# Kernel optimization log

Measured on AMD Instinct MI355X. Metric: run time of the kernel, lower is better.

The kernel has to match this reference:

```python
import jax, jax.numpy as jnp
import numpy as np

N_NODES = 100_000
N_EDGES = 1_600_000
N_SPECIES = 4
ATTR = 16
HID = 32
NBASIS = 8
SH = 4  # l=0 (1) + l=1 (3)
R_CUT = 5.0


def setup_inputs() -> dict:
    key = jax.random.key(0)
    ks = jax.random.split(key, 13)
    inp = {
        "x": jax.random.randint(ks[0], (N_NODES,), 0, N_SPECIES),
        "pos": jax.random.normal(ks[1], (N_NODES, 3), jnp.float32),
        "edge_index": jax.random.randint(ks[2], (2, N_EDGES), 0, N_NODES),
        "cell": jax.random.normal(ks[3], (3, 3), jnp.float32),
        "cell_offset": jax.random.randint(ks[4], (N_EDGES, 3), 0, 3),
        "elem_embed": jax.random.normal(ks[5], (N_SPECIES, ATTR), jnp.float32),
        "W_embed": jax.random.normal(ks[6], (ATTR, HID), jnp.float32) * 0.25,
        "Wr": jax.random.normal(ks[7], (3, NBASIS, HID * SH), jnp.float32) * 0.25,
        "br": jax.random.normal(ks[8], (3, HID * SH), jnp.float32) * 0.1,
        "Wout": jax.random.normal(ks[9], (3, HID, HID), jnp.float32) * 0.18,
        "Wsc": jax.random.normal(ks[10], (3, ATTR, HID), jnp.float32) * 0.25,
        "P1": jax.random.normal(ks[11], (HID, 32), jnp.float32) * 0.18,
        "P2": jax.random.normal(ks[12], (32, 4), jnp.float32) * 0.18,
    }
    return inp


def _radial_basis(r, r_safe):
    # Bessel basis with smooth polynomial cutoff (p = 6)
    n = jnp.arange(1, NBASIS + 1, dtype=r.dtype)  # [NBASIS]
    rb = jnp.sin(n * jnp.pi * r / R_CUT) / r_safe  # [E, NBASIS]
    u = r / R_CUT
    p = 6.0
    env = 1.0 - (p + 1) * (p + 2) / 2 * u ** p + p * (p + 2) * u ** (p + 1) - p * (p + 1) / 2 * u ** (p + 2)
    env = jnp.where(u < 1.0, env, 0.0)
    return rb * env


def reference(x, pos, edge_index, cell, cell_offset, elem_embed, W_embed, Wr, br, Wout, Wsc, P1, P2):
    src, dst = edge_index[0], edge_index[1]
    n_nodes = pos.shape[0]
    n_edges = src.shape[0]

    # PBC shift vectors (offsets in {-1,0,1})
    period_vec = (cell_offset.astype(pos.dtype) - 1.0) @ cell  # [E,3]

    # node attributes / initial embedding
    x_attr = elem_embed[x]          # [N, ATTR]
    h = x_attr @ W_embed            # [N, HID]

    # edge attributes: vectors, lengths, spherical harmonics (l<=1)
    edge_vec = pos[dst] - pos[src] + period_vec            # [E,3]
    r = jnp.linalg.norm(edge_vec, axis=-1, keepdims=True)  # [E,1]
    r_safe = jnp.maximum(r, 1e-9)
    unit = edge_vec / r_safe
    edge_sh = jnp.concatenate([jnp.ones_like(r), unit], axis=-1)  # [E,SH]

    rbf = _radial_basis(r, r_safe)  # [E, NBASIS]

    # 3 message-passing convolutions
    for l in range(3):
        w = (rbf @ Wr[l] + br[l]).reshape(n_edges, HID, SH)          # per-edge TP weights
        msg = jnp.einsum('eh,es,ehs->eh', h[src], edge_sh, w)        # gather + edge compute
        agg = jax.ops.segment_sum(msg, dst, num_segments=n_nodes)    # scatter-reduce
        h = jax.nn.silu(agg @ Wout[l] + x_attr @ Wsc[l])

    # post-conv readout
    h = jax.nn.silu(h @ P1) @ P2  # [N,4]
    energies = h[:, 0]
    forces = h[:, 1:4]
    return energies, forces
```

## Files before the change

kernel.cpp:

```cpp
#include <hip/hip_runtime.h>
#include <hip/hip_bf16.h>
#include <math.h>

#define NN 100000
#define NE 1600000
#define HIDD 32
#define ATTR_ 16
#define NB 8
#define NBUK 782
#define BCAP 4096
#define SCHUNK 4096

typedef __hip_bfloat16 bf16;
typedef _Float16 half8  __attribute__((ext_vector_type(8)));
typedef _Float16 half2v __attribute__((ext_vector_type(2)));
typedef float    f32x4  __attribute__((ext_vector_type(4)));

__device__ __forceinline__ float silu_(float v){ return v / (1.f + expf(-v)); }

__global__ void k_init(const int* __restrict__ x, const float* __restrict__ elem,
                       const float* __restrict__ Wemb, bf16* __restrict__ h,
                       float* __restrict__ agg){
  int idx = blockIdx.x*256 + threadIdx.x;
  if (idx >= NN*HIDD) return;
  int node = idx >> 5, hh = idx & 31;
  int xi = x[node];
  float acc = 0.f;
  #pragma unroll
  for (int a=0; a<ATTR_; a++) acc += elem[xi*ATTR_+a] * Wemb[a*HIDD+hh];
  h[idx] = __float2bfloat16(acc);
  agg[idx] = 0.f;
}

__global__ void k_bzero(int* __restrict__ bcnt){
  int i = blockIdx.x*1024 + threadIdx.x;
  if (i < NBUK) bcnt[i] = 0;
}

__global__ void __launch_bounds__(256) k_bhist(const int* __restrict__ ei,
                                               int* __restrict__ bcnt){
  __shared__ int lh[NBUK];
  const int t = threadIdx.x;
  for (int i=t; i<NBUK; i+=256) lh[i] = 0;
  __syncthreads();
  const size_t base = (size_t)blockIdx.x * 8192;
  #pragma unroll
  for (int k=0; k<32; k++){
    size_t e = base + (size_t)k*256 + t;
    if (e < NE) atomicAdd(&lh[ei[NE + e] >> 7], 1);
  }
  __syncthreads();
  for (int i=t; i<NBUK; i+=256){ int v = lh[i]; if (v) atomicAdd(&bcnt[i], v); }
}

__global__ void __launch_bounds__(1024) k_bscan(const int* __restrict__ bcnt,
                                                int* __restrict__ boff,
                                                int* __restrict__ bcur){
  __shared__ int s[1024];
  const int t = threadIdx.x;
  int v = (t < NBUK) ? bcnt[t] : 0;
  s[t] = v; __syncthreads();
  #pragma unroll
  for (int off=1; off<1024; off<<=1){
    int u = (t >= off) ? s[t-off] : 0;
    __syncthreads();
    s[t] += u;
    __syncthreads();
  }
  int ex = s[t] - v;
  if (t < NBUK){ boff[t] = ex; bcur[t] = ex; }
  if (t == NBUK-1) boff[NBUK] = s[t];
}

__global__ void __launch_bounds__(256) k_bscatter(
    const int* __restrict__ ei, const int* __restrict__ coff,
    int* __restrict__ bcur, int* __restrict__ pairs){
  __shared__ int lh[NBUK];
  __shared__ int gb[NBUK];
  __shared__ int sbr[SCHUNK];
  __shared__ int spay[SCHUNK];
  const int t = threadIdx.x;
  const int base = blockIdx.x * SCHUNK;
  for (int i=t; i<NBUK; i+=256) lh[i] = 0;
  __syncthreads();
  for (int rr=0; rr<SCHUNK; rr+=256){
    int e = base + rr + t;
    if (e < NE){
      int src = ei[e], dst = ei[NE + e];
      int code = coff[e*3+0] + 3*coff[e*3+1] + 9*coff[e*3+2];
      int b = dst >> 7;
      int rank = atomicAdd(&lh[b], 1);
      sbr[rr+t]  = (b<<16) | rank;
      spay[rr+t] = src | (code<<17) | ((dst & 127)<<22);
    }
  }
  __syncthreads();
  for (int i=t; i<NBUK; i+=256){
    int c = lh[i];
    gb[i] = c ? atomicAdd(&bcur[i], c) : 0;
  }
  __syncthreads();
  for (int rr=0; rr<SCHUNK; rr+=256){
    int e = base + rr + t;
    if (e < NE){
      int br = sbr[rr+t];
      pairs[gb[br>>16] + (br & 0xFFFF)] = spay[rr+t];
    }
  }
}

__global__ void __launch_bounds__(256) k_fsort(
    const int* __restrict__ pairs, const int* __restrict__ boff,
    int* __restrict__ es, int* __restrict__ dsts){
  __shared__ int spay[BCAP];
  __shared__ int hist[128];
  __shared__ int cur[128];
  const int b = blockIdx.x, t = threadIdx.x;
  const int base = boff[b];
  int K = boff[b+1] - base;
  if (K > BCAP) K = BCAP;
  if (t < 128) hist[t] = 0;
  __syncthreads();
  for (int i=t; i<K; i+=256){
    int pay = pairs[base + i];
    spay[i] = pay;
    atomicAdd(&hist[(pay>>22) & 127], 1);
  }
  __syncthreads();
  if (t < 128) cur[t] = hist[t];
  __syncthreads();
  #pragma unroll
  for (int off=1; off<128; off<<=1){
    int u = (t >= off && t < 128) ? cur[t-off] : 0;
    __syncthreads();
    if (t < 128) cur[t] += u;
    __syncthreads();
  }
  if (t < 128) cur[t] -= hist[t];
  __syncthreads();
  const int node0 = b << 7;
  for (int i=t; i<K; i+=256){
    int pay = spay[i];
    int loc = (pay>>22) & 127;
    int p = base + atomicAdd(&cur[loc], 1);
    es[p]   = pay;
    dsts[p] = node0 + loc;
  }
}

__global__ void __launch_bounds__(256) k_edge4(
    const int* __restrict__ es, const int* __restrict__ dsts,
    const float* __restrict__ pos, const float* __restrict__ cell,
    const float* __restrict__ Wr_l, const float* __restrict__ br_l,
    const bf16* __restrict__ h, float* __restrict__ agg){
  __shared__ _Float16 Gs[256][40];
  __shared__ float ssh[256][4];
  __shared__ int ssrc[256];
  __shared__ int sdst[256];
  __shared__ _Float16 W2T[32][32];
  __shared__ float scell[9];
  const int t = threadIdx.x;
  if (t < 9) scell[t] = cell[t];
  {
    int hh2 = t >> 3, kq = t & 7;
    float4 w4 = *reinterpret_cast<const float4*>(Wr_l + kq*128 + hh2*4);
    W2T[hh2][kq*4+0] = (_Float16)w4.x;
    W2T[hh2][kq*4+1] = (_Float16)w4.y;
    W2T[hh2][kq*4+2] = (_Float16)w4.z;
    W2T[hh2][kq*4+3] = (_Float16)w4.w;
  }
  __syncthreads();

  {
    const int j = blockIdx.x*256 + t;
    int pay = es[j];
    int dst = dsts[j];
    int src  = pay & 0x1FFFF;
    int code = (pay >> 17) & 31;
    ssrc[t] = src; sdst[t] = dst;
    int q = code / 3;
    float c0 = (float)(code - 3*q - 1);
    float c1 = (float)(q - 3*(q/3) - 1);
    float c2 = (float)(q/3 - 1);
    float vx = pos[dst*3+0]-pos[src*3+0] + c0*scell[0]+c1*scell[3]+c2*scell[6];
    float vy = pos[dst*3+1]-pos[src*3+1] + c0*scell[1]+c1*scell[4]+c2*scell[7];
    float vz = pos[dst*3+2]-pos[src*3+2] + c0*scell[2]+c1*scell[5]+c2*scell[8];
    float r  = sqrtf(vx*vx + vy*vy + vz*vz);
    float rs = fmaxf(r, 1e-9f);
    float u  = r * 0.2f;
    float env = 0.f;
    if (u < 1.f){
      float u2=u*u, u3=u2*u, u6=u3*u3, u7=u6*u, u8=u7*u;
      env = 1.f - 28.f*u6 + 48.f*u7 - 21.f*u8;
    }
    float sc = env / rs;
    float s1, c1t;
    __sincosf(0.62831853071795864769f * r, &s1, &c1t);
    float twoc = 2.f*c1t;
    float inv = 1.f / rs;
    float ux = vx*inv, uy = vy*inv, uz = vz*inv;
    float sp = 0.f, sn = s1;
    #pragma unroll
    for (int b=0; b<NB; b++){
      float rb = sn*sc;
      half2v p0 = { (_Float16)rb,      (_Float16)(rb*ux) };
      half2v p1 = { (_Float16)(rb*uy), (_Float16)(rb*uz) };
      *reinterpret_cast<half2v*>(&Gs[t][b*4])   = p0;
      *reinterpret_cast<half2v*>(&Gs[t][b*4+2]) = p1;
      float nx = twoc*sn - sp; sp = sn; sn = nx;
    }
    float4 sh4 = make_float4(1.f, ux, uy, uz);
    *reinterpret_cast<float4*>(ssh[t]) = sh4;
  }
  __syncthreads();

  {
    const int w = t >> 6, l = t & 63;
    const int lrow = l & 15, lk = l >> 4;
    half8 b0 = *reinterpret_cast<half8*>(&W2T[lrow][lk*8]);
    half8 b1 = *reinterpret_cast<half8*>(&W2T[16+lrow][lk*8]);
    float4 br0 = *reinterpret_cast<const float4*>(br_l + 4*lrow);
    float4 br1 = *reinterpret_cast<const float4*>(br_l + 4*(16+lrow));
    f32x4 acc[4][2];
    const f32x4 zz = {0.f,0.f,0.f,0.f};
    #pragma unroll
    for (int m=0; m<4; m++){
      int row = (w*4+m)*16 + lrow;
      half8 a = *reinterpret_cast<half8*>(&Gs[row][lk*8]);
      acc[m][0] = __builtin_amdgcn_mfma_f32_16x16x32_f16(a, b0, zz, 0, 0, 0);
      acc[m][1] = __builtin_amdgcn_mfma_f32_16x16x32_f16(a, b1, zz, 0, 0, 0);
    }
    #pragma unroll
    for (int m=0; m<4; m++){
      #pragma unroll
      for (int r=0; r<4; r++){
        int edge = (w*4+m)*16 + lk*4 + r;
        float4 sh4 = *reinterpret_cast<float4*>(ssh[edge]);
        float bias0 = sh4.x*br0.x + sh4.y*br0.y + sh4.z*br0.z + sh4.w*br0.w;
        float bias1 = sh4.x*br1.x + sh4.y*br1.y + sh4.z*br1.z + sh4.w*br1.w;
        Gs[edge][lrow]    = (_Float16)(acc[m][0][r] + bias0);
        Gs[edge][16+lrow] = (_Float16)(acc[m][1][r] + bias1);
      }
    }
  }
  __syncthreads();

  const int g = t >> 5, hh = t & 31, base = g*32;
  float accv = 0.f;
  int cur = sdst[base];
  float buf[16];
  #pragma unroll
  for (int half = 0; half < 2; half++){
    const int kb = base + half*16;
    #pragma unroll
    for (int k=0; k<16; k++)
      buf[k] = __bfloat162float(h[(size_t)ssrc[kb+k]*HIDD + hh]);
    #pragma unroll
    for (int k=0; k<16; k++){
      const int idx = kb + k;
      int dst = sdst[idx];
      if (dst != cur){ atomicAdd(agg + (size_t)cur*HIDD + hh, accv); accv = 0.f; cur = dst; }
      float cv = (float)Gs[idx][hh];
      accv += buf[k]*cv;
    }
  }
  atomicAdd(agg + (size_t)cur*HIDD + hh, accv);
}

__global__ void __launch_bounds__(256) k_edge(
    const float* __restrict__ pos, const int* __restrict__ ei,
    const float* __restrict__ cell, const int* __restrict__ coff,
    const float* __restrict__ Wr_l, const float* __restrict__ br_l,
    const bf16* __restrict__ h, float* __restrict__ agg){
  __shared__ float sfeat[8][12];
  __shared__ int   snode[8][2];
  const int e0 = blockIdx.x * 8;
  const int t  = threadIdx.x;
  if (t < 8){
    int e = e0 + t;
    int src = ei[e], dst = ei[NE + e];
    snode[t][0] = src; snode[t][1] = dst;
    float c0 = (float)(coff[e*3+0] - 1);
    float c1 = (float)(coff[e*3+1] - 1);
    float c2 = (float)(coff[e*3+2] - 1);
    float vx = pos[dst*3+0]-pos[src*3+0] + c0*cell[0]+c1*cell[3]+c2*cell[6];
    float vy = pos[dst*3+1]-pos[src*3+1] + c0*cell[1]+c1*cell[4]+c2*cell[7];
    float vz = pos[dst*3+2]-pos[src*3+2] + c0*cell[2]+c1*cell[5]+c2*cell[8];
    float r  = sqrtf(vx*vx+vy*vy+vz*vz);
    float rs = fmaxf(r, 1e-9f);
    float u  = r * 0.2f;
    float env = 0.f;
    if (u < 1.f){
      float u2=u*u, u3=u2*u, u6=u3*u3, u7=u6*u, u8=u7*u;
      env = 1.f - 28.f*u6 + 48.f*u7 - 21.f*u8;
    }
    float sc = env / rs;
    #pragma unroll
    for (int b=0; b<NB; b++)
      sfeat[t][b] = sinf((float)(b+1) * 3.14159265358979323846f * u) * sc;
    float inv = 1.f / rs;
    sfeat[t][8]  = 1.f;
    sfeat[t][9]  = vx*inv;
    sfeat[t][10] = vy*inv;
    sfeat[t][11] = vz*inv;
  }
  __syncthreads();
  const int el = t >> 5, hh = t & 31;
  const int src = snode[el][0], dst = snode[el][1];
  float hs = __bfloat162float(h[(size_t)src*HIDD + hh]);
  float4 acc = *reinterpret_cast<const float4*>(br_l + 4*hh);
  #pragma unroll
  for (int b=0; b<NB; b++){
    float rb = sfeat[el][b];
    float4 w = *reinterpret_cast<const float4*>(Wr_l + b*128 + 4*hh);
    acc.x += rb*w.x; acc.y += rb*w.y; acc.z += rb*w.z; acc.w += rb*w.w;
  }
  float c = acc.x*sfeat[el][8] + acc.y*sfeat[el][9]
          + acc.z*sfeat[el][10] + acc.w*sfeat[el][11];
  atomicAdd(agg + (size_t)dst*HIDD + hh, hs*c);
}

__global__ void k_node(const int* __restrict__ x, const float* __restrict__ elem,
                       const float* __restrict__ Wout_l, const float* __restrict__ Wsc_l,
                       bf16* __restrict__ h, float* __restrict__ agg){
  int idx = blockIdx.x*256 + threadIdx.x;
  if (idx >= NN*HIDD) return;
  int node = idx >> 5, hh = idx & 31;
  int xi = x[node];
  const float* arow = agg + (size_t)node*HIDD;
  float acc = 0.f;
  #pragma unroll
  for (int i=0; i<HIDD; i++) acc += arow[i] * Wout_l[i*HIDD+hh];
  #pragma unroll
  for (int a=0; a<ATTR_; a++) acc += elem[xi*ATTR_+a] * Wsc_l[a*HIDD+hh];
  h[idx] = __float2bfloat16(silu_(acc));
  agg[idx] = 0.f;
}

__global__ void __launch_bounds__(256) k_final2(
    const bf16* __restrict__ h, const float* __restrict__ P1,
    const float* __restrict__ P2, float* __restrict__ out){
  __shared__ float sP1[32][32];
  __shared__ float sh[8][32];
  const int t = threadIdx.x;
  {
    float4 v = reinterpret_cast<const float4*>(P1)[t];
    int r = (t*4) >> 5, c = (t*4) & 31;
    sP1[r][c]   = v.x; sP1[r][c+1] = v.y;
    sP1[r][c+2] = v.z; sP1[r][c+3] = v.w;
  }
  const int node0 = blockIdx.x * 8;
  ((float*)sh)[t] = __bfloat162float(h[(size_t)node0*HIDD + t]);
  __syncthreads();
  const int g = t >> 5, j = t & 31;
  const int node = node0 + g;
  float tj = 0.f;
  #pragma unroll
  for (int i=0; i<32; i++) tj += sh[g][i] * sP1[i][j];
  tj = silu_(tj);
  float4 p2 = reinterpret_cast<const float4*>(P2)[j];
  float o0 = tj*p2.x, o1 = tj*p2.y, o2 = tj*p2.z, o3 = tj*p2.w;
  #pragma unroll
  for (int m=1; m<32; m<<=1){
    o0 += __shfl_xor(o0, m);
    o1 += __shfl_xor(o1, m);
    o2 += __shfl_xor(o2, m);
    o3 += __shfl_xor(o3, m);
  }
  if (j == 0){
    out[node]            = o0;
    out[NN + node*3 + 0] = o1;
    out[NN + node*3 + 1] = o2;
    out[NN + node*3 + 2] = o3;
  }
}

extern "C" void kernel_launch(void* const* d_in, const int* in_sizes, int n_in,
                              void* d_out, int out_size, void* d_ws, size_t ws_size,
                              hipStream_t stream){
  const int*   x    = (const int*)  d_in[0];
  const float* pos  = (const float*)d_in[1];
  const int*   ei   = (const int*)  d_in[2];
  const float* cell = (const float*)d_in[3];
  const int*   coff = (const int*)  d_in[4];
  const float* elem = (const float*)d_in[5];
  const float* Wemb = (const float*)d_in[6];
  const float* Wr   = (const float*)d_in[7];
  const float* br   = (const float*)d_in[8];
  const float* Wout = (const float*)d_in[9];
  const float* Wsc  = (const float*)d_in[10];
  const float* P1   = (const float*)d_in[11];
  const float* P2   = (const float*)d_in[12];
  float* out = (float*)d_out;

  char* w = (char*)d_ws;
  bf16*  h    = (bf16*)w;  w += (size_t)NN*HIDD*2;
  float* agg  = (float*)w; w += (size_t)NN*HIDD*4;
  int*   cnt  = (int*)w;   w += (size_t)NN*4;
  int*   es   = (int*)w;   w += (size_t)NE*4;
  int*   dsts = (int*)w;   w += (size_t)NE*4;
  const size_t need = (size_t)(w - (char*)d_ws);
  const bool fast = (ws_size >= need);
  int* boff = cnt;
  int* bcur = cnt + 1024;
  int* bcnt = cnt + 2048;
  int* pairs = (int*)agg;

  if (fast){
    k_bzero<<<1, 1024, 0, stream>>>(bcnt);
    k_bhist<<<(NE + 8191)/8192, 256, 0, stream>>>(ei, bcnt);
    k_bscan<<<1, 1024, 0, stream>>>(bcnt, boff, bcur);
    k_bscatter<<<(NE + SCHUNK-1)/SCHUNK, 256, 0, stream>>>(ei, coff, bcur, pairs);
    k_fsort<<<NBUK, 256, 0, stream>>>(pairs, boff, es, dsts);
  }
  k_init<<<(NN*HIDD+255)/256, 256, 0, stream>>>(x, elem, Wemb, h, agg);
  for (int l=0; l<3; l++){
    if (fast){
      k_edge4<<<NE/256, 256, 0, stream>>>(es, dsts, pos, cell,
                                          Wr + (size_t)l*NB*HIDD*4, br + (size_t)l*HIDD*4,
                                          h, agg);
    } else {
      k_edge<<<NE/8, 256, 0, stream>>>(pos, ei, cell, coff,
                                       Wr + (size_t)l*NB*HIDD*4, br + (size_t)l*HIDD*4,
                                       h, agg);
    }
    k_node<<<(NN*HIDD+255)/256, 256, 0, stream>>>(x, elem,
                                       Wout + (size_t)l*HIDD*HIDD, Wsc + (size_t)l*ATTR_*HIDD,
                                       h, agg);
  }
  k_final2<<<NN/8, 256, 0, stream>>>(h, P1, P2, out);
}
```

Measured before the change: 344.8 us.

## Prefetch h gathers early, drop a barrier, and swizzle blocks per XCD

The edge kernel now issues the 32 per-thread bf16 h gathers and the pos loads right after reading the edge indices, so their latency overlaps the radial-basis and MFMA work. The barrier between the MFMA write-back and the accumulate phase is removed; this relies on each wave consuming only the Gs rows it wrote itself. Block indices are remapped so consecutive dst-sorted blocks land on the same XCD, to improve L2 locality for the agg atomics. The cost is higher register pressure from holding 32 prefetched values per thread.

New measurement: 341.6 us. Within noise of the previous version (-1.0%).

```diff
diff --git a/kernel.cpp b/kernel.cpp
--- a/kernel.cpp
+++ b/kernel.cpp
@@ -148,7 +148,7 @@
   }
 }
 
-__global__ void __launch_bounds__(256) k_edge4(
+__global__ void __launch_bounds__(256) k_edge5(
     const int* __restrict__ es, const int* __restrict__ dsts,
     const float* __restrict__ pos, const float* __restrict__ cell,
     const float* __restrict__ Wr_l, const float* __restrict__ br_l,
@@ -160,6 +160,15 @@
   __shared__ _Float16 W2T[32][32];
   __shared__ float scell[9];
   const int t = threadIdx.x;
+
+  int blk;
+  {
+    const int nwg = gridDim.x;
+    int q = nwg >> 3, r = nwg & 7;
+    int xcd = blockIdx.x & 7, lidx = blockIdx.x >> 3;
+    blk = (xcd < r) ? (xcd*(q+1) + lidx) : (r*(q+1) + (xcd-r)*q + lidx);
+  }
+
   if (t < 9) scell[t] = cell[t];
   {
     int hh2 = t >> 3, kq = t & 7;
@@ -169,22 +178,32 @@
     W2T[hh2][kq*4+2] = (_Float16)w4.z;
     W2T[hh2][kq*4+3] = (_Float16)w4.w;
   }
-  __syncthreads();
+
+  const int j = blk*256 + t;
+  const int pay = es[j];
+  const int dstn = dsts[j];
+  const int srcn = pay & 0x1FFFF;
+  ssrc[t] = srcn; sdst[t] = dstn;
+  float pdx = pos[dstn*3+0], pdy = pos[dstn*3+1], pdz = pos[dstn*3+2];
+  float psx = pos[srcn*3+0], psy = pos[srcn*3+1], psz = pos[srcn*3+2];
+  __syncthreads();
+
+  const int g = t >> 5, hh = t & 31, base = g*32;
+  const unsigned short* hu = reinterpret_cast<const unsigned short*>(h);
+  unsigned short hb[32];
+  #pragma unroll
+  for (int k=0; k<32; k++)
+    hb[k] = hu[(size_t)ssrc[base+k]*HIDD + hh];
 
   {
-    const int j = blockIdx.x*256 + t;
-    int pay = es[j];
-    int dst = dsts[j];
-    int src  = pay & 0x1FFFF;
     int code = (pay >> 17) & 31;
-    ssrc[t] = src; sdst[t] = dst;
     int q = code / 3;
     float c0 = (float)(code - 3*q - 1);
     float c1 = (float)(q - 3*(q/3) - 1);
     float c2 = (float)(q/3 - 1);
-    float vx = pos[dst*3+0]-pos[src*3+0] + c0*scell[0]+c1*scell[3]+c2*scell[6];
-    float vy = pos[dst*3+1]-pos[src*3+1] + c0*scell[1]+c1*scell[4]+c2*scell[7];
-    float vz = pos[dst*3+2]-pos[src*3+2] + c0*scell[2]+c1*scell[5]+c2*scell[8];
+    float vx = pdx - psx + c0*scell[0]+c1*scell[3]+c2*scell[6];
+    float vy = pdy - psy + c0*scell[1]+c1*scell[4]+c2*scell[7];
+    float vz = pdz - psz + c0*scell[2]+c1*scell[5]+c2*scell[8];
     float r  = sqrtf(vx*vx + vy*vy + vz*vz);
     float rs = fmaxf(r, 1e-9f);
     float u  = r * 0.2f;
@@ -212,7 +231,10 @@
     float4 sh4 = make_float4(1.f, ux, uy, uz);
     *reinterpret_cast<float4*>(ssh[t]) = sh4;
   }
-  __syncthreads();
+
+  asm volatile("s_waitcnt lgkmcnt(0)" ::: "memory");
+  __builtin_amdgcn_s_barrier();
+  __builtin_amdgcn_sched_barrier(0);
 
   {
     const int w = t >> 6, l = t & 63;
@@ -221,48 +243,34 @@
     half8 b1 = *reinterpret_cast<half8*>(&W2T[16+lrow][lk*8]);
     float4 br0 = *reinterpret_cast<const float4*>(br_l + 4*lrow);
     float4 br1 = *reinterpret_cast<const float4*>(br_l + 4*(16+lrow));
-    f32x4 acc[4][2];
     const f32x4 zz = {0.f,0.f,0.f,0.f};
     #pragma unroll
     for (int m=0; m<4; m++){
       int row = (w*4+m)*16 + lrow;
       half8 a = *reinterpret_cast<half8*>(&Gs[row][lk*8]);
-      acc[m][0] = __builtin_amdgcn_mfma_f32_16x16x32_f16(a, b0, zz, 0, 0, 0);
-      acc[m][1] = __builtin_amdgcn_mfma_f32_16x16x32_f16(a, b1, zz, 0, 0, 0);
-    }
-    #pragma unroll
-    for (int m=0; m<4; m++){
+      f32x4 c0 = __builtin_amdgcn_mfma_f32_16x16x32_f16(a, b0, zz, 0, 0, 0);
+      f32x4 c1 = __builtin_amdgcn_mfma_f32_16x16x32_f16(a, b1, zz, 0, 0, 0);
       #pragma unroll
       for (int r=0; r<4; r++){
         int edge = (w*4+m)*16 + lk*4 + r;
         float4 sh4 = *reinterpret_cast<float4*>(ssh[edge]);
         float bias0 = sh4.x*br0.x + sh4.y*br0.y + sh4.z*br0.z + sh4.w*br0.w;
         float bias1 = sh4.x*br1.x + sh4.y*br1.y + sh4.z*br1.z + sh4.w*br1.w;
-        Gs[edge][lrow]    = (_Float16)(acc[m][0][r] + bias0);
-        Gs[edge][16+lrow] = (_Float16)(acc[m][1][r] + bias1);
+        Gs[edge][lrow]    = (_Float16)(c0[r] + bias0);
+        Gs[edge][16+lrow] = (_Float16)(c1[r] + bias1);
       }
     }
   }
-  __syncthreads();
-
-  const int g = t >> 5, hh = t & 31, base = g*32;
+
   float accv = 0.f;
   int cur = sdst[base];
-  float buf[16];
-  #pragma unroll
-  for (int half = 0; half < 2; half++){
-    const int kb = base + half*16;
-    #pragma unroll
-    for (int k=0; k<16; k++)
-      buf[k] = __bfloat162float(h[(size_t)ssrc[kb+k]*HIDD + hh]);
-    #pragma unroll
-    for (int k=0; k<16; k++){
-      const int idx = kb + k;
-      int dst = sdst[idx];
-      if (dst != cur){ atomicAdd(agg + (size_t)cur*HIDD + hh, accv); accv = 0.f; cur = dst; }
-      float cv = (float)Gs[idx][hh];
-      accv += buf[k]*cv;
-    }
+  #pragma unroll
+  for (int k=0; k<32; k++){
+    const int idx = base + k;
+    int dst = sdst[idx];
+    if (dst != cur){ atomicAdd(agg + (size_t)cur*HIDD + hh, accv); accv = 0.f; cur = dst; }
+    float hv = __uint_as_float(((unsigned)hb[k]) << 16);
+    accv += hv * (float)Gs[idx][hh];
   }
   atomicAdd(agg + (size_t)cur*HIDD + hh, accv);
 }
@@ -416,7 +424,7 @@
   k_init<<<(NN*HIDD+255)/256, 256, 0, stream>>>(x, elem, Wemb, h, agg);
   for (int l=0; l<3; l++){
     if (fast){
-      k_edge4<<<NE/256, 256, 0, stream>>>(es, dsts, pos, cell,
+      k_edge5<<<NE/256, 256, 0, stream>>>(es, dsts, pos, cell,
                                           Wr + (size_t)l*NB*HIDD*4, br + (size_t)l*HIDD*4,
                                           h, agg);
     } else {
```
